# Kernel optimization log

Hardware: AMD Instinct MI355X
Metric: run time of the kernel (lower is better)

Reference implementation:

```python
import jax, jax.numpy as jnp
import numpy as np

B, S, D, L, H = 8, 1024, 512, 6, 8
HD = D // H


def setup_inputs() -> dict:
    key = jax.random.key(0)
    sc = D ** -0.5
    inp = {
        "xr": jax.random.normal(jax.random.fold_in(key, 0), (B, S, D), jnp.float32),
        "xi": jax.random.normal(jax.random.fold_in(key, 1), (B, S, D), jnp.float32),
    }
    wnames = ["Wq_r", "Wq_i", "Wk_r", "Wk_i", "Wv_r", "Wv_i", "Wo_r", "Wo_i",
              "W1_r", "W1_i", "W2_r", "W2_i"]
    for i, n in enumerate(wnames):
        inp[n] = jax.random.normal(jax.random.fold_in(key, 10 + i), (L, D, D), jnp.float32) * sc
    for n in ["bq_r", "bq_i", "bk_r", "bk_i", "bv_r", "bv_i", "bo_r", "bo_i",
              "b1_r", "b1_i", "b2_r", "b2_i"]:
        inp[n] = jnp.zeros((L, D), jnp.float32)
    g0 = 1.0 / np.sqrt(2.0)  # standard complex-LN affine init
    for n in ["ln1_grr", "ln1_gii", "ln2_grr", "ln2_gii"]:
        inp[n] = jnp.full((L, D), g0, jnp.float32)
    for n in ["ln1_gri", "ln1_br", "ln1_bi", "ln2_gri", "ln2_br", "ln2_bi"]:
        inp[n] = jnp.zeros((L, D), jnp.float32)
    return inp


def clin(xr, xi, Wr, Wi, br, bi):
    # ComplexLinear: (xr + i xi)(Wr + i Wi)^T + (br + i bi)
    yr = xr @ Wr.T - xi @ Wi.T + br
    yi = xr @ Wi.T + xi @ Wr.T + bi
    return yr, yi


def cln(xr, xi, grr, gri, gii, br, bi, eps=1e-5):
    # Complex LayerNorm: 2x2 covariance whitening over the feature dim + affine
    mr = xr.mean(-1, keepdims=True)
    mi = xi.mean(-1, keepdims=True)
    cr, ci = xr - mr, xi - mi
    Vrr = (cr * cr).mean(-1, keepdims=True) + eps
    Vii = (ci * ci).mean(-1, keepdims=True) + eps
    Vri = (cr * ci).mean(-1, keepdims=True)
    s = jnp.sqrt(Vrr * Vii - Vri * Vri)
    t = jnp.sqrt(Vrr + Vii + 2.0 * s)
    st = s * t
    Wrr = (Vii + s) / st
    Wii = (Vrr + s) / st
    Wri = -Vri / st
    hr = Wrr * cr + Wri * ci
    hi = Wri * cr + Wii * ci
    return grr * hr + gri * hi + br, gri * hr + gii * hi + bi


def reference(xr, xi,
              Wq_r, Wq_i, bq_r, bq_i, Wk_r, Wk_i, bk_r, bk_i,
              Wv_r, Wv_i, bv_r, bv_i, Wo_r, Wo_i, bo_r, bo_i,
              W1_r, W1_i, b1_r, b1_i, W2_r, W2_i, b2_r, b2_i,
              ln1_grr, ln1_gri, ln1_gii, ln1_br, ln1_bi,
              ln2_grr, ln2_gri, ln2_gii, ln2_br, ln2_bi):
    b, s, d = xr.shape
    nl = Wq_r.shape[0]
    h = H
    hd = d // h
    scale = hd ** -0.5
    for l in range(nl):
        rr, ri = xr, xi
        qr, qi = clin(xr, xi, Wq_r[l], Wq_i[l], bq_r[l], bq_i[l])
        kr, ki = clin(xr, xi, Wk_r[l], Wk_i[l], bk_r[l], bk_i[l])
        vr, vi = clin(xr, xi, Wv_r[l], Wv_i[l], bv_r[l], bv_i[l])
        split = lambda a: a.reshape(b, s, h, hd)
        qr, qi, kr, ki, vr, vi = map(split, (qr, qi, kr, ki, vr, vi))
        # sm_variante='real': softmax over Re(q k^H) = qr.kr + qi.ki
        logits = (jnp.einsum('bqhd,bkhd->bhqk', qr, kr)
                  + jnp.einsum('bqhd,bkhd->bhqk', qi, ki)) * scale
        A = jax.nn.softmax(logits, axis=-1)  # real-valued attention weights
        o_r = jnp.einsum('bhqk,bkhd->bqhd', A, vr).reshape(b, s, d)
        o_i = jnp.einsum('bhqk,bkhd->bqhd', A, vi).reshape(b, s, d)
        o_r, o_i = clin(o_r, o_i, Wo_r[l], Wo_i[l], bo_r[l], bo_i[l])
        xr, xi = o_r + rr, o_i + ri
        xr, xi = cln(xr, xi, ln1_grr[l], ln1_gri[l], ln1_gii[l], ln1_br[l], ln1_bi[l])
        rr, ri = xr, xi
        hr, hi = clin(xr, xi, W1_r[l], W1_i[l], b1_r[l], b1_i[l])
        hr, hi = jax.nn.relu(hr), jax.nn.relu(hi)  # CReLU; dropout = identity (eval)
        hr, hi = clin(hr, hi, W2_r[l], W2_i[l], b2_r[l], b2_i[l])
        xr, xi = hr + rr, hi + ri
        xr, xi = cln(xr, xi, ln2_grr[l], ln2_gri[l], ln2_gii[l], ln2_br[l], ln2_bi[l])
    return jnp.stack([xr, xi])  # [2, B, S, D] (real, imag)
```

## Files before the change

kernel.cpp:

```cpp
#include <hip/hip_runtime.h>
#include <cstddef>
#include <cstdint>

constexpr int NB   = 8;
constexpr int SEQ  = 1024;
constexpr int DIM  = 512;
constexpr int NL   = 6;
constexpr int NH   = 8;
constexpr int HDIM = 64;
constexpr int ROWS = NB * SEQ;
constexpr size_t BSD = (size_t)ROWS * DIM;
constexpr int KHAT = 1024;

typedef __attribute__((ext_vector_type(8))) short bfrag;
typedef __attribute__((ext_vector_type(4))) float f32x4;
typedef __attribute__((ext_vector_type(4))) unsigned short us4;

__device__ __forceinline__ void f4a(const float4 v, float* a) {
    a[0] = v.x; a[1] = v.y; a[2] = v.z; a[3] = v.w;
}
__device__ __forceinline__ float4 a4f(const float* a) {
    float4 v; v.x = a[0]; v.y = a[1]; v.z = a[2]; v.w = a[3]; return v;
}
__device__ __forceinline__ unsigned short f2bf(float f) {
    union { float f; uint32_t u; } x{f};
    return (unsigned short)((x.u + 0x7fffu + ((x.u >> 16) & 1u)) >> 16);
}
__device__ __forceinline__ float bf2f(unsigned short u) {
    union { uint32_t u; float f; } x;
    x.u = (uint32_t)u << 16;
    return x.f;
}
__device__ __forceinline__ uint32_t cvtpk(float lo, float hi) {
    uint32_t r;
    asm("v_cvt_pk_bf16_f32 %0, %1, %2" : "=v"(r) : "v"(lo), "v"(hi));
    return r;
}
__device__ __forceinline__ void gload16(const unsigned short* g, void* l) {
    __builtin_amdgcn_global_load_lds(
        (const __attribute__((address_space(1))) void*)g,
        (__attribute__((address_space(3))) void*)l, 16, 0, 0);
}

struct PrepArgs {
    const float* Wr[6]; const float* Wi[6];
    const float* br[6]; const float* bi[6];
};

__global__ __launch_bounds__(256)
void prep_kernel(PrepArgs a, unsigned short* __restrict__ Ball,
                 float* __restrict__ biasall, int layer)
{
    const int lin = blockIdx.y;
    const int nh_ = blockIdx.x;
    const float* Wr = a.Wr[lin] + (size_t)layer * DIM * DIM;
    const float* Wi = a.Wi[lin] + (size_t)layer * DIM * DIM;

    bool real; int n0;
    if (lin < 3) { const int dh = nh_ & 127; real = dh < 64; n0 = (nh_ >> 7) * 64 + (dh & 63); }
    else         { real = nh_ < 512; n0 = nh_ & 511; }

    const int t = threadIdx.x;
    const int kk = (t * 4) & 511;
    const bool fh = t < 128;
    const float* src;
    float sgn = 1.f;
    if (fh) src = real ? Wr : Wi;
    else { if (real) { src = Wi; sgn = -1.f; } else src = Wr; }

    float v[4];
    f4a(*(const float4*)(src + (size_t)n0 * 512 + kk), v);
    us4 o;
    #pragma unroll
    for (int j = 0; j < 4; ++j) o[j] = f2bf(sgn * v[j]);
    *(us4*)(Ball + (size_t)lin * KHAT * KHAT + (size_t)nh_ * KHAT + t * 4) = o;
    if (t == 0)
        biasall[lin * KHAT + nh_] = real ? a.br[lin][layer * DIM + n0]
                                         : a.bi[lin][layer * DIM + n0];
}

__global__ __launch_bounds__(256)
void gemm_qkv(const unsigned short* __restrict__ Xh,
              const unsigned short* __restrict__ Ball,
              const float* __restrict__ biasall,
              unsigned short* __restrict__ Qh,
              unsigned short* __restrict__ Kh,
              unsigned short* __restrict__ Vth)
{
    __shared__ __align__(16) unsigned short Asm[128 * 32];
    __shared__ __align__(16) unsigned short Bsm[128 * 32];

    const int t = threadIdx.x, lane = t & 63, w = t >> 6;
    const int wm = w >> 1, wn = w & 1;
    const int c = lane & 15, g = lane >> 4;

    int bid = blockIdx.y * 24 + blockIdx.x;
    bid = (bid & 7) * 192 + (bid >> 3);
    const int nblk = bid % 24, mblk = bid / 24;
    const int n0g = nblk * 128;
    const int m0 = mblk * 128;
    const int lin = n0g >> 10;
    const int n0 = n0g & 1023;
    const unsigned short* Bh = Ball + (size_t)lin * KHAT * KHAT;
    const float* bias = biasall + lin * KHAT;

    f32x4 acc[4][4];
    #pragma unroll
    for (int i = 0; i < 4; ++i)
        #pragma unroll
        for (int j = 0; j < 4; ++j) acc[i][j] = (f32x4){0.f, 0.f, 0.f, 0.f};

    const int srow = (w << 4) + (lane >> 2);
    const int scol = (lane & 3) * 8;
    const unsigned short* gA0 = Xh + (size_t)(m0 + srow) * KHAT + scol;
    const unsigned short* gA1 = Xh + (size_t)(m0 + 64 + srow) * KHAT + scol;
    const unsigned short* gB0 = Bh + (size_t)(n0 + srow) * KHAT + scol;
    const unsigned short* gB1 = Bh + (size_t)(n0 + 64 + srow) * KHAT + scol;
    char* aBase = (char*)Asm + (w << 10);
    char* bBase = (char*)Bsm + (w << 10);

    for (int ks = 0; ks < 32; ++ks) {
        const int k0 = ks * 32;
        __syncthreads();
        gload16(gA0 + k0, aBase);
        gload16(gA1 + k0, aBase + 4096);
        gload16(gB0 + k0, bBase);
        gload16(gB1 + k0, bBase + 4096);
        __syncthreads();

        bfrag af[4], bf2[4];
        #pragma unroll
        for (int mi = 0; mi < 4; ++mi)
            af[mi] = *(const bfrag*)(Asm + (wm * 64 + mi * 16 + c) * 32 + g * 8);
        #pragma unroll
        for (int ni = 0; ni < 4; ++ni)
            bf2[ni] = *(const bfrag*)(Bsm + (wn * 64 + ni * 16 + c) * 32 + g * 8);
        #pragma unroll
        for (int mi = 0; mi < 4; ++mi)
            #pragma unroll
            for (int ni = 0; ni < 4; ++ni)
                acc[mi][ni] = __builtin_amdgcn_mfma_f32_16x16x32_bf16(
                    af[mi], bf2[ni], acc[mi][ni], 0, 0, 0);
    }

    const int mbase = m0 + wm * 64;
    const int nbase = n0 + wn * 64;
    unsigned short* dqk = (lin == 0) ? Qh : Kh;
    #pragma unroll
    for (int mi = 0; mi < 4; ++mi) {
        #pragma unroll
        for (int ni = 0; ni < 4; ++ni) {
            const int n = nbase + ni * 16 + c;
            const float bv = bias[n];
            float v[4];
            #pragma unroll
            for (int r = 0; r < 4; ++r) v[r] = acc[mi][ni][r] + bv;
            const int mrow = mbase + mi * 16 + g * 4;
            const int b = mrow >> 10, s = mrow & 1023;
            const int h = n >> 7, dh = n & 127;
            if (lin < 2) {
                const size_t a = ((size_t)(b * NH + h) * SEQ + s) * 128 + dh;
                #pragma unroll
                for (int r = 0; r < 4; ++r) dqk[a + (size_t)r * 128] = f2bf(v[r]);
            } else {
                const int ck = (s & 31) >> 2;
                const int sp = (s & ~31) | ((((ck & 3) << 1) | (ck >> 2)) << 2);
                const size_t a = ((size_t)(b * NH + h) * 128 + dh) * SEQ + sp;
                us4 o;
                #pragma unroll
                for (int r = 0; r < 4; ++r) o[r] = f2bf(v[r]);
                *(us4*)(Vth + a) = o;
            }
        }
    }
}

template <bool RELU>
__global__ __launch_bounds__(256)
void gemm_mfma(const unsigned short* __restrict__ Xh,
               const unsigned short* __restrict__ Bh,
               const float* __restrict__ bias,
               unsigned short* __restrict__ Yh)
{
    __shared__ __align__(16) unsigned short Asm[128 * 32];
    __shared__ __align__(16) unsigned short Bsm[128 * 32];

    const int t = threadIdx.x, lane = t & 63, w = t >> 6;
    const int wm = w >> 1, wn = w & 1;
    const int c = lane & 15, g = lane >> 4;

    int bid = blockIdx.y * 8 + blockIdx.x;
    bid = (bid & 7) * 64 + (bid >> 3);
    const int n0 = (bid & 7) * 128;
    const int m0 = (bid >> 3) * 128;

    f32x4 acc[4][4];
    #pragma unroll
    for (int i = 0; i < 4; ++i)
        #pragma unroll
        for (int j = 0; j < 4; ++j) acc[i][j] = (f32x4){0.f, 0.f, 0.f, 0.f};

    const int srow = (w << 4) + (lane >> 2);
    const int scol = (lane & 3) * 8;
    const unsigned short* gA0 = Xh + (size_t)(m0 + srow) * KHAT + scol;
    const unsigned short* gA1 = Xh + (size_t)(m0 + 64 + srow) * KHAT + scol;
    const unsigned short* gB0 = Bh + (size_t)(n0 + srow) * KHAT + scol;
    const unsigned short* gB1 = Bh + (size_t)(n0 + 64 + srow) * KHAT + scol;
    char* aBase = (char*)Asm + (w << 10);
    char* bBase = (char*)Bsm + (w << 10);

    for (int ks = 0; ks < 32; ++ks) {
        const int k0 = ks * 32;
        __syncthreads();
        gload16(gA0 + k0, aBase);
        gload16(gA1 + k0, aBase + 4096);
        gload16(gB0 + k0, bBase);
        gload16(gB1 + k0, bBase + 4096);
        __syncthreads();

        bfrag af[4], bf2[4];
        #pragma unroll
        for (int mi = 0; mi < 4; ++mi)
            af[mi] = *(const bfrag*)(Asm + (wm * 64 + mi * 16 + c) * 32 + g * 8);
        #pragma unroll
        for (int ni = 0; ni < 4; ++ni)
            bf2[ni] = *(const bfrag*)(Bsm + (wn * 64 + ni * 16 + c) * 32 + g * 8);
        #pragma unroll
        for (int mi = 0; mi < 4; ++mi)
            #pragma unroll
            for (int ni = 0; ni < 4; ++ni)
                acc[mi][ni] = __builtin_amdgcn_mfma_f32_16x16x32_bf16(
                    af[mi], bf2[ni], acc[mi][ni], 0, 0, 0);
    }

    const int mbase = m0 + wm * 64;
    const int nbase = n0 + wn * 64;
    #pragma unroll
    for (int mi = 0; mi < 4; ++mi) {
        #pragma unroll
        for (int ni = 0; ni < 4; ++ni) {
            const int n = nbase + ni * 16 + c;
            const float bv = bias[n];
            const int mrow = mbase + mi * 16 + g * 4;
            #pragma unroll
            for (int r = 0; r < 4; ++r) {
                float v = acc[mi][ni][r] + bv;
                if (RELU) v = fmaxf(v, 0.f);
                Yh[(size_t)(mrow + r) * KHAT + n] = f2bf(v);
            }
        }
    }
}

__global__ __launch_bounds__(256)
void attn_mfma(const unsigned short* __restrict__ Qh,
               const unsigned short* __restrict__ Kh,
               const unsigned short* __restrict__ Vth,
               unsigned short* __restrict__ Ah)
{
    __shared__ __align__(16) char smem[32768];
    char* Ksm = smem;
    char* Vsm = smem + 16384;
    const int t    = threadIdx.x;
    const int lane = t & 63;
    const int wv   = t >> 6;
    const int c    = lane & 15;
    const int g    = lane >> 4;

    int bid = blockIdx.x + 16 * blockIdx.y + 128 * blockIdx.z;
    bid = (bid & 7) * 128 + (bid >> 3);
    const int q0 = (bid & 15) * 64;
    const int bh = bid >> 4;
    const int hh = bh & 7, bb = bh >> 3;
    const size_t qkb = (size_t)bh * SEQ * 128;
    const size_t vtb = (size_t)bh * 128 * SEQ;

    constexpr float SC  = 0.125f * 1.44269504f;
    constexpr float THR = 11.0f;

    bfrag qf[4];
    {
        const unsigned short* qp = Qh + qkb + (size_t)(q0 + wv * 16 + c) * 128 + g * 8;
        #pragma unroll
        for (int ks = 0; ks < 4; ++ks) qf[ks] = *(const bfrag*)(qp + ks * 32);
    }

    f32x4 oacc[8];
    #pragma unroll
    for (int i = 0; i < 8; ++i) oacc[i] = (f32x4){0.f, 0.f, 0.f, 0.f};
    float mrun = -1e30f, lrun = 0.f;

    const int kkey = t >> 2, kq = t & 3;
    const unsigned short* kgp = Kh + qkb + (size_t)kkey * 128 + kq * 32;
    const int vd = t >> 1, vh2 = t & 1;
    const unsigned short* vgp = Vth + vtb + (size_t)vd * SEQ + vh2 * 32;

    bfrag krg[4], vrg[4];
    #pragma unroll
    for (int j = 0; j < 4; ++j) krg[j] = *(const bfrag*)(kgp + j * 8);
    #pragma unroll
    for (int j = 0; j < 4; ++j) vrg[j] = *(const bfrag*)(vgp + j * 8);

    for (int k0 = 0; k0 < SEQ; k0 += 64) {
        __syncthreads();
        #pragma unroll
        for (int j = 0; j < 4; ++j) {
            const int boff = (kkey * 256 + (kq * 32 + j * 8) * 2) ^ ((kkey & 7) << 4);
            *(bfrag*)(Ksm + boff) = krg[j];
        }
        #pragma unroll
        for (int j = 0; j < 4; ++j) {
            const int boff = (vd * 128 + (vh2 * 32 + j * 8) * 2) ^ ((vd & 7) << 4);
            *(bfrag*)(Vsm + boff) = vrg[j];
        }
        __syncthreads();

        if (k0 + 64 < SEQ) {
            const int kn = k0 + 64;
            #pragma unroll
            for (int j = 0; j < 4; ++j) krg[j] = *(const bfrag*)(kgp + (size_t)kn * 128 + j * 8);
            #pragma unroll
            for (int j = 0; j < 4; ++j) vrg[j] = *(const bfrag*)(vgp + kn + j * 8);
        }

        f32x4 sa[4];
        #pragma unroll
        for (int nt = 0; nt < 4; ++nt) sa[nt] = (f32x4){0.f, 0.f, 0.f, 0.f};
        __builtin_amdgcn_s_setprio(1);
        #pragma unroll
        for (int nt = 0; nt < 4; ++nt) {
            const int key = nt * 16 + c;
            #pragma unroll
            for (int ks = 0; ks < 4; ++ks) {
                const int boff = (key * 256 + (ks * 32 + g * 8) * 2) ^ ((key & 7) << 4);
                const bfrag bk = *(const bfrag*)(Ksm + boff);
                sa[nt] = __builtin_amdgcn_mfma_f32_16x16x32_bf16(bk, qf[ks], sa[nt], 0, 0, 0);
            }
        }
        __builtin_amdgcn_s_setprio(0);

        float sv[4][4];
        #pragma unroll
        for (int nt = 0; nt < 4; ++nt)
            #pragma unroll
            for (int r = 0; r < 4; ++r) sv[nt][r] = sa[nt][r] * SC;

        float mloc = sv[0][0];
        #pragma unroll
        for (int nt = 0; nt < 4; ++nt)
            #pragma unroll
            for (int r = 0; r < 4; ++r) mloc = fmaxf(mloc, sv[nt][r]);
        if (__any(mloc > mrun + THR)) {
            float mt = mloc;
            mt = fmaxf(mt, __shfl_xor(mt, 16, 64));
            mt = fmaxf(mt, __shfl_xor(mt, 32, 64));
            const float mn = fmaxf(mrun, mt);
            const float fs = exp2f(mrun - mn);
            mrun = mn;
            lrun *= fs;
            #pragma unroll
            for (int i = 0; i < 8; ++i) {
                oacc[i][0] *= fs; oacc[i][1] *= fs; oacc[i][2] *= fs; oacc[i][3] *= fs;
            }
        }

        float p[4][4];
        float psum = 0.f;
        #pragma unroll
        for (int nt = 0; nt < 4; ++nt)
            #pragma unroll
            for (int r = 0; r < 4; ++r) {
                p[nt][r] = exp2f(sv[nt][r] - mrun);
                psum += p[nt][r];
            }
        psum += __shfl_xor(psum, 16, 64);
        psum += __shfl_xor(psum, 32, 64);
        lrun += psum;

        uint32_t pk0[4], pk1[4];
        #pragma unroll
        for (int nt = 0; nt < 4; ++nt) {
            pk0[nt] = cvtpk(p[nt][0], p[nt][1]);
            pk1[nt] = cvtpk(p[nt][2], p[nt][3]);
        }

        __builtin_amdgcn_s_setprio(1);
        #pragma unroll
        for (int k2 = 0; k2 < 2; ++k2) {
            union { uint32_t u[4]; bfrag f; } pb;
            pb.u[0] = pk0[2 * k2];
            pb.u[1] = pk1[2 * k2];
            pb.u[2] = pk0[2 * k2 + 1];
            pb.u[3] = pk1[2 * k2 + 1];
            const int kb2 = (k2 * 32 + g * 8) * 2;
            #pragma unroll
            for (int mtl = 0; mtl < 8; ++mtl) {
                const int d = mtl * 16 + c;
                const bfrag va = *(const bfrag*)(Vsm + ((d * 128 + kb2) ^ ((d & 7) << 4)));
                oacc[mtl] = __builtin_amdgcn_mfma_f32_16x16x32_bf16(va, pb.f, oacc[mtl], 0, 0, 0);
            }
        }
        __builtin_amdgcn_s_setprio(0);
    }

    {
        const float ic = 1.0f / lrun;
        #pragma unroll
        for (int i = 0; i < 8; ++i) {
            oacc[i][0] *= ic; oacc[i][1] *= ic; oacc[i][2] *= ic; oacc[i][3] *= ic;
        }
    }
    __syncthreads();
    float* Ox = (float*)(smem + wv * 8192);
    #pragma unroll
    for (int mtl = 0; mtl < 8; ++mtl)
        #pragma unroll
        for (int r = 0; r < 4; ++r)
            Ox[(mtl * 16 + 4 * g + r) * 16 + c] = oacc[mtl][r];
    asm volatile("s_waitcnt lgkmcnt(0)" ::: "memory");
    __builtin_amdgcn_sched_barrier(0);

    const int q = lane >> 2, qt = lane & 3;
    const int colbase = (qt >> 1) * 512 + hh * 64 + (qt & 1) * 32;
    const size_t rowm = (size_t)bb * SEQ + q0 + wv * 16 + q;
    unsigned short* dst = Ah + rowm * KHAT + colbase;
    #pragma unroll
    for (int j = 0; j < 8; ++j) {
        us4 o;
        #pragma unroll
        for (int e = 0; e < 4; ++e) o[e] = f2bf(Ox[(qt * 32 + j * 4 + e) * 16 + q]);
        *(us4*)(dst + j * 4) = o;
    }
}

__global__ __launch_bounds__(256)
void cln_kernel(const unsigned short* __restrict__ U,
                float* __restrict__ Xr, float* __restrict__ Xi,
                unsigned short* __restrict__ Xh,
                const float* __restrict__ Grr, const float* __restrict__ Gri,
                const float* __restrict__ Gii, const float* __restrict__ Bbr,
                const float* __restrict__ Bbi)
{
    const int lane = threadIdx.x & 63;
    const int row  = blockIdx.x * 4 + (threadIdx.x >> 6);
    const size_t off = (size_t)row * DIM;
    const int c0 = lane * 4;
    const int c1 = 256 + lane * 4;

    float xr[8], xi[8];
    {
        const unsigned short* up = U + (size_t)row * KHAT;
        us4 a0 = *(const us4*)(up + c0);
        us4 a1 = *(const us4*)(up + c1);
        us4 b0 = *(const us4*)(up + 512 + c0);
        us4 b1 = *(const us4*)(up + 512 + c1);
        float t0[4], t1[4];
        f4a(*(const float4*)&Xr[off + c0], t0);
        f4a(*(const float4*)&Xr[off + c1], t1);
        #pragma unroll
        for (int j = 0; j < 4; ++j) { xr[j] = bf2f(a0[j]) + t0[j]; xr[4 + j] = bf2f(a1[j]) + t1[j]; }
        f4a(*(const float4*)&Xi[off + c0], t0);
        f4a(*(const float4*)&Xi[off + c1], t1);
        #pragma unroll
        for (int j = 0; j < 4; ++j) { xi[j] = bf2f(b0[j]) + t0[j]; xi[4 + j] = bf2f(b1[j]) + t1[j]; }
    }

    float sr = 0.f, si = 0.f, srr = 0.f, sii = 0.f, sri = 0.f;
    #pragma unroll
    for (int j = 0; j < 8; ++j) {
        sr += xr[j]; si += xi[j];
        srr = fmaf(xr[j], xr[j], srr);
        sii = fmaf(xi[j], xi[j], sii);
        sri = fmaf(xr[j], xi[j], sri);
    }
    #pragma unroll
    for (int m = 32; m >= 1; m >>= 1) {
        sr  += __shfl_xor(sr,  m, 64);
        si  += __shfl_xor(si,  m, 64);
        srr += __shfl_xor(srr, m, 64);
        sii += __shfl_xor(sii, m, 64);
        sri += __shfl_xor(sri, m, 64);
    }

    const float inv_d = 1.0f / DIM;
    const float mr = sr * inv_d, mi = si * inv_d;
    const float Vrr = srr * inv_d - mr * mr + 1e-5f;
    const float Vii = sii * inv_d - mi * mi + 1e-5f;
    const float Vri = sri * inv_d - mr * mi;
    const float s  = sqrtf(Vrr * Vii - Vri * Vri);
    const float tt = sqrtf(Vrr + Vii + 2.0f * s);
    const float ist = 1.0f / (s * tt);
    const float Wrr = (Vii + s) * ist;
    const float Wii = (Vrr + s) * ist;
    const float Wri = -Vri * ist;

    #pragma unroll
    for (int half = 0; half < 2; ++half) {
        const int c = half ? c1 : c0;
        float grr[4], gri[4], gii[4], pbr[4], pbi[4];
        f4a(*(const float4*)&Grr[c], grr);
        f4a(*(const float4*)&Gri[c], gri);
        f4a(*(const float4*)&Gii[c], gii);
        f4a(*(const float4*)&Bbr[c], pbr);
        f4a(*(const float4*)&Bbi[c], pbi);
        float outr[4], outi[4];
        #pragma unroll
        for (int j = 0; j < 4; ++j) {
            const int idx = half * 4 + j;
            const float cr = xr[idx] - mr;
            const float ci = xi[idx] - mi;
            const float hr = Wrr * cr + Wri * ci;
            const float hi = Wri * cr + Wii * ci;
            outr[j] = fmaf(grr[j], hr, fmaf(gri[j], hi, pbr[j]));
            outi[j] = fmaf(gri[j], hr, fmaf(gii[j], hi, pbi[j]));
        }
        *(float4*)&Xr[off + c] = a4f(outr);
        *(float4*)&Xi[off + c] = a4f(outi);
        us4 hr_, hi_;
        #pragma unroll
        for (int j = 0; j < 4; ++j) { hr_[j] = f2bf(outr[j]); hi_[j] = f2bf(outi[j]); }
        *(us4*)(Xh + (size_t)row * KHAT + c)       = hr_;
        *(us4*)(Xh + (size_t)row * KHAT + 512 + c) = hi_;
    }
}

__global__ __launch_bounds__(256)
void init_cvt(const float* __restrict__ xr, const float* __restrict__ xi,
              float* __restrict__ outr, float* __restrict__ outi,
              unsigned short* __restrict__ Xh)
{
    const size_t i = ((size_t)blockIdx.x * 256 + threadIdx.x) * 4;
    float vr[4], vi[4];
    f4a(*(const float4*)(xr + i), vr);
    f4a(*(const float4*)(xi + i), vi);
    *(float4*)(outr + i) = a4f(vr);
    *(float4*)(outi + i) = a4f(vi);
    const size_t m = i >> 9;
    const int k = (int)(i & 511);
    us4 a, b;
    #pragma unroll
    for (int j = 0; j < 4; ++j) { a[j] = f2bf(vr[j]); b[j] = f2bf(vi[j]); }
    *(us4*)(Xh + m * KHAT + k)       = a;
    *(us4*)(Xh + m * KHAT + 512 + k) = b;
}

extern "C" void kernel_launch(void* const* d_in, const int* in_sizes, int n_in,
                              void* d_out, int out_size, void* d_ws, size_t ws_size,
                              hipStream_t stream) {
    (void)in_sizes; (void)n_in; (void)out_size; (void)ws_size;

    const float* in_xr = (const float*)d_in[0];
    const float* in_xi = (const float*)d_in[1];
    PrepArgs pa;
    pa.Wr[0] = (const float*)d_in[2];  pa.Wi[0] = (const float*)d_in[3];
    pa.Wr[1] = (const float*)d_in[4];  pa.Wi[1] = (const float*)d_in[5];
    pa.Wr[2] = (const float*)d_in[6];  pa.Wi[2] = (const float*)d_in[7];
    pa.Wr[3] = (const float*)d_in[8];  pa.Wi[3] = (const float*)d_in[9];
    pa.Wr[4] = (const float*)d_in[10]; pa.Wi[4] = (const float*)d_in[11];
    pa.Wr[5] = (const float*)d_in[12]; pa.Wi[5] = (const float*)d_in[13];
    pa.br[0] = (const float*)d_in[14]; pa.bi[0] = (const float*)d_in[15];
    pa.br[1] = (const float*)d_in[16]; pa.bi[1] = (const float*)d_in[17];
    pa.br[2] = (const float*)d_in[18]; pa.bi[2] = (const float*)d_in[19];
    pa.br[3] = (const float*)d_in[20]; pa.bi[3] = (const float*)d_in[21];
    pa.br[4] = (const float*)d_in[22]; pa.bi[4] = (const float*)d_in[23];
    pa.br[5] = (const float*)d_in[24]; pa.bi[5] = (const float*)d_in[25];
    const float* ln1_grr = (const float*)d_in[26];
    const float* ln1_gii = (const float*)d_in[27];
    const float* ln2_grr = (const float*)d_in[28];
    const float* ln2_gii = (const float*)d_in[29];
    const float* ln1_gri = (const float*)d_in[30];
    const float* ln1_br  = (const float*)d_in[31];
    const float* ln1_bi  = (const float*)d_in[32];
    const float* ln2_gri = (const float*)d_in[33];
    const float* ln2_br  = (const float*)d_in[34];
    const float* ln2_bi  = (const float*)d_in[35];

    float* outr = (float*)d_out;
    float* outi = outr + BSD;

    char* ws = (char*)d_ws;
    unsigned short* Xh  = (unsigned short*)(ws);
    unsigned short* Qh  = (unsigned short*)(ws + 16777216);
    unsigned short* Kh  = (unsigned short*)(ws + 2 * 16777216);
    unsigned short* Vth = (unsigned short*)(ws + 3 * 16777216);
    unsigned short* Ah  = (unsigned short*)(ws + 4 * 16777216);
    unsigned short* Ball = (unsigned short*)(ws + 5 * 16777216);
    float* biasall = (float*)(ws + 5 * 16777216 + 12582912);
    unsigned short* Uh = Kh;
    unsigned short* Hh = Qh;

    init_cvt<<<ROWS * DIM / 1024, 256, 0, stream>>>(in_xr, in_xi, outr, outi, Xh);

    const dim3 pgrid(KHAT, 6);
    const dim3 qgrid(24, ROWS / 128);
    const dim3 ggrid(KHAT / 128, ROWS / 128);
    const dim3 agrid(SEQ / 64, NH, NB);
    const int  lgrid = ROWS / 4;

    for (int l = 0; l < NL; ++l) {
        const size_t bo = (size_t)l * DIM;
        prep_kernel<<<pgrid, 256, 0, stream>>>(pa, Ball, biasall, l);

        unsigned short* Bo = Ball + (size_t)3 * KHAT * KHAT;
        unsigned short* B1 = Ball + (size_t)4 * KHAT * KHAT;
        unsigned short* B2 = Ball + (size_t)5 * KHAT * KHAT;

        gemm_qkv<<<qgrid, 256, 0, stream>>>(Xh, Ball, biasall, Qh, Kh, Vth);
        attn_mfma<<<agrid, 256, 0, stream>>>(Qh, Kh, Vth, Ah);
        gemm_mfma<false><<<ggrid, 256, 0, stream>>>(Ah, Bo, biasall + 3 * KHAT, Uh);
        cln_kernel<<<lgrid, 256, 0, stream>>>(Uh, outr, outi, Xh,
                                              ln1_grr + bo, ln1_gri + bo, ln1_gii + bo,
                                              ln1_br + bo, ln1_bi + bo);
        gemm_mfma<true><<<ggrid, 256, 0, stream>>>(Xh, B1, biasall + 4 * KHAT, Hh);
        gemm_mfma<false><<<ggrid, 256, 0, stream>>>(Hh, B2, biasall + 5 * KHAT, Uh);
        cln_kernel<<<lgrid, 256, 0, stream>>>(Uh, outr, outi, Xh,
                                              ln2_grr + bo, ln2_gri + bo, ln2_gii + bo,
                                              ln2_br + bo, ln2_bi + bo);
    }
}
```

Before: 1.522 ms.

## Load K fragments directly from global in attention and fold softmax scale into Q

Attention no longer stages K tiles through shared memory. Each wave now loads its K MFMA fragments straight from global memory, with a one-tile-ahead register prefetch across the four key subtiles. The softmax scale (1/sqrt(hd)·log2e) moves into the Q projection epilogue, which removes the per-score multiply. The trade-off is that every wave reads K redundantly from global/L2 instead of sharing it through LDS, and the Q values are rounded to bf16 after scaling.

```diff
diff --git a/kernel.cpp b/kernel.cpp
--- a/kernel.cpp
+++ b/kernel.cpp
@@ -41,6 +41,8 @@
         (const __attribute__((address_space(1))) void*)g,
         (__attribute__((address_space(3))) void*)l, 16, 0, 0);
 }
+
+constexpr float ATT_SC = 0.125f * 1.44269504f;
 
 struct PrepArgs {
     const float* Wr[6]; const float* Wi[6];
@@ -154,7 +156,10 @@
             const float bv = bias[n];
             float v[4];
             #pragma unroll
-            for (int r = 0; r < 4; ++r) v[r] = acc[mi][ni][r] + bv;
+            for (int r = 0; r < 4; ++r) {
+                v[r] = acc[mi][ni][r] + bv;
+                if (lin == 0) v[r] *= ATT_SC;
+            }
             const int mrow = mbase + mi * 16 + g * 4;
             const int b = mrow >> 10, s = mrow & 1023;
             const int h = n >> 7, dh = n & 127;
@@ -259,8 +264,7 @@
                unsigned short* __restrict__ Ah)
 {
     __shared__ __align__(16) char smem[32768];
-    char* Ksm = smem;
-    char* Vsm = smem + 16384;
+    char* Vsm = smem;
     const int t    = threadIdx.x;
     const int lane = t & 63;
     const int wv   = t >> 6;
@@ -275,7 +279,6 @@
     const size_t qkb = (size_t)bh * SEQ * 128;
     const size_t vtb = (size_t)bh * 128 * SEQ;
 
-    constexpr float SC  = 0.125f * 1.44269504f;
     constexpr float THR = 11.0f;
 
     bfrag qf[4];
@@ -290,24 +293,22 @@
     for (int i = 0; i < 8; ++i) oacc[i] = (f32x4){0.f, 0.f, 0.f, 0.f};
     float mrun = -1e30f, lrun = 0.f;
 
-    const int kkey = t >> 2, kq = t & 3;
-    const unsigned short* kgp = Kh + qkb + (size_t)kkey * 128 + kq * 32;
+    const unsigned short* kbase = Kh + qkb + (size_t)c * 128 + g * 8;
+
     const int vd = t >> 1, vh2 = t & 1;
     const unsigned short* vgp = Vth + vtb + (size_t)vd * SEQ + vh2 * 32;
 
-    bfrag krg[4], vrg[4];
-    #pragma unroll
-    for (int j = 0; j < 4; ++j) krg[j] = *(const bfrag*)(kgp + j * 8);
+    bfrag vrg[4];
     #pragma unroll
     for (int j = 0; j < 4; ++j) vrg[j] = *(const bfrag*)(vgp + j * 8);
 
     for (int k0 = 0; k0 < SEQ; k0 += 64) {
+        bfrag kcur[4], knxt[4];
+        #pragma unroll
+        for (int ks = 0; ks < 4; ++ks)
+            kcur[ks] = *(const bfrag*)(kbase + (size_t)k0 * 128 + ks * 32);
+
         __syncthreads();
-        #pragma unroll
-        for (int j = 0; j < 4; ++j) {
-            const int boff = (kkey * 256 + (kq * 32 + j * 8) * 2) ^ ((kkey & 7) << 4);
-            *(bfrag*)(Ksm + boff) = krg[j];
-        }
         #pragma unroll
         for (int j = 0; j < 4; ++j) {
             const int boff = (vd * 128 + (vh2 * 32 + j * 8) * 2) ^ ((vd & 7) << 4);
@@ -318,38 +319,34 @@
         if (k0 + 64 < SEQ) {
             const int kn = k0 + 64;
             #pragma unroll
-            for (int j = 0; j < 4; ++j) krg[j] = *(const bfrag*)(kgp + (size_t)kn * 128 + j * 8);
-            #pragma unroll
             for (int j = 0; j < 4; ++j) vrg[j] = *(const bfrag*)(vgp + kn + j * 8);
         }
 
         f32x4 sa[4];
         #pragma unroll
-        for (int nt = 0; nt < 4; ++nt) sa[nt] = (f32x4){0.f, 0.f, 0.f, 0.f};
-        __builtin_amdgcn_s_setprio(1);
-        #pragma unroll
         for (int nt = 0; nt < 4; ++nt) {
-            const int key = nt * 16 + c;
-            #pragma unroll
-            for (int ks = 0; ks < 4; ++ks) {
-                const int boff = (key * 256 + (ks * 32 + g * 8) * 2) ^ ((key & 7) << 4);
-                const bfrag bk = *(const bfrag*)(Ksm + boff);
-                sa[nt] = __builtin_amdgcn_mfma_f32_16x16x32_bf16(bk, qf[ks], sa[nt], 0, 0, 0);
-            }
-        }
-        __builtin_amdgcn_s_setprio(0);
-
-        float sv[4][4];
+            if (nt < 3) {
+                #pragma unroll
+                for (int ks = 0; ks < 4; ++ks)
+                    knxt[ks] = *(const bfrag*)(kbase + (size_t)(k0 + (nt + 1) * 16) * 128 + ks * 32);
+            }
+            sa[nt] = (f32x4){0.f, 0.f, 0.f, 0.f};
+            __builtin_amdgcn_s_setprio(1);
+            #pragma unroll
+            for (int ks = 0; ks < 4; ++ks)
+                sa[nt] = __builtin_amdgcn_mfma_f32_16x16x32_bf16(kcur[ks], qf[ks], sa[nt], 0, 0, 0);
+            __builtin_amdgcn_s_setprio(0);
+            if (nt < 3) {
+                #pragma unroll
+                for (int ks = 0; ks < 4; ++ks) kcur[ks] = knxt[ks];
+            }
+        }
+
+        float mloc = sa[0][0];
         #pragma unroll
         for (int nt = 0; nt < 4; ++nt)
             #pragma unroll
-            for (int r = 0; r < 4; ++r) sv[nt][r] = sa[nt][r] * SC;
-
-        float mloc = sv[0][0];
-        #pragma unroll
-        for (int nt = 0; nt < 4; ++nt)
-            #pragma unroll
-            for (int r = 0; r < 4; ++r) mloc = fmaxf(mloc, sv[nt][r]);
+            for (int r = 0; r < 4; ++r) mloc = fmaxf(mloc, sa[nt][r]);
         if (__any(mloc > mrun + THR)) {
             float mt = mloc;
             mt = fmaxf(mt, __shfl_xor(mt, 16, 64));
@@ -370,7 +367,7 @@
         for (int nt = 0; nt < 4; ++nt)
             #pragma unroll
             for (int r = 0; r < 4; ++r) {
-                p[nt][r] = exp2f(sv[nt][r] - mrun);
+                p[nt][r] = exp2f(sa[nt][r] - mrun);
                 psum += p[nt][r];
             }
         psum += __shfl_xor(psum, 16, 64);
```

Result: slower. 1.878 ms (+23.4%).
